# Kernel tuning notes

Measured on AMD Instinct MI355X. Metric: run time of the kernel, lower is better.

The kernel has to match this reference:

```python
import jax, jax.numpy as jnp
import numpy as np
from jax import lax

N_TOKENS = 524288
N_EXPERTS = 64
TOP_K = 8


def setup_inputs() -> dict:
    key = jax.random.key(0)
    logits = jax.random.normal(key, (N_TOKENS, N_EXPERTS), dtype=jnp.float32)
    # expert_counts / assignments / offsets are output buffers in the torch
    # module (filled by the custom kernel); pass zero placeholders.
    return {
        "expert_counts": jnp.zeros((N_EXPERTS,), dtype=jnp.int32),
        "assignments": jnp.zeros((N_TOKENS, TOP_K), dtype=jnp.int32),
        "offsets": jnp.zeros((N_TOKENS, TOP_K), dtype=jnp.int32),
        "logits": logits,
    }


def reference(expert_counts, assignments, offsets, logits):
    """Ragged top-k gating (replay_routing=False).

    Returns (expert_counts, scores, assignments, offsets, logits_out):
      scores       [N, K]  top-k softmax probabilities per token
      assignments  [N, K]  top-k expert ids per token
      offsets      [N, K]  slot of each (token, k) within its expert's
                           ragged bucket (token-major arrival order)
      expert_counts[E]     number of routed slots per expert
      logits_out           pass-through copy of logits
    """
    N, E = logits.shape
    K = assignments.shape[1]

    probs = jax.nn.softmax(logits, axis=-1)            # [N, E]
    scores, assign = lax.top_k(probs, K)               # [N, K] each
    assign = assign.astype(jnp.int32)

    flat = assign.reshape(-1)                          # [N*K], token-major
    counts = jnp.zeros((E,), jnp.int32).at[flat].add(1)

    # offsets: rank of each slot among equal-expert slots in arrival order.
    # Stable sort by expert id; within-expert rank = sorted position minus
    # the expert's segment start (exclusive cumsum of counts).
    order = jnp.argsort(flat, stable=True)             # [N*K]
    sorted_e = flat[order]
    starts = jnp.concatenate(
        [jnp.zeros((1,), jnp.int32), jnp.cumsum(counts)[:-1].astype(jnp.int32)]
    )                                                  # [E]
    ranks = jnp.arange(N * K, dtype=jnp.int32) - starts[sorted_e]
    offs = jnp.zeros((N * K,), jnp.int32).at[order].set(ranks).reshape(N, K)

    return counts, scores, assign, offs, logits
```

## Files before the change

kernel.cpp:

```cpp
#include <hip/hip_runtime.h>

#define NT 524288
#define NE 64
#define NK 8
#define TPB 128
#define NBLK (NT / TPB)
#define SPB (TPB * NK)

__global__ __launch_bounds__(256) void topk_kernel(
    const float* __restrict__ logits,
    float* __restrict__ out_scores,
    float* __restrict__ out_assign,
    float* __restrict__ out_logits,
    int* __restrict__ blockCounts)
{
    __shared__ int wcnt[4][NE];

    const int t = threadIdx.x;
    const int b = blockIdx.x;
    const int g = t & 7;
    const int tok_in_pass = t >> 3;
    const int w = t >> 6;
    const int l = t & 63;
    const unsigned long long lt_mask = (l == 0) ? 0ull : ((~0ull) >> (64 - l));

    int myCount = 0;

    for (int pass = 0; pass < 4; ++pass) {
        const int ltok = pass * 32 + tok_in_pass;
        const int token = b * TPB + ltok;
        const float* lp = logits + (size_t)token * NE + g * 8;
        float4 v0 = *(const float4*)lp;
        float4 v1 = *(const float4*)(lp + 4);
        float* op = out_logits + (size_t)token * NE + g * 8;
        *(float4*)op = v0;
        *(float4*)(op + 4) = v1;

        float lv[8] = {v0.x, v0.y, v0.z, v0.w, v1.x, v1.y, v1.z, v1.w};

        float m = lv[0];
        #pragma unroll
        for (int j = 1; j < 8; ++j) m = fmaxf(m, lv[j]);
        #pragma unroll
        for (int sh = 1; sh < 8; sh <<= 1) m = fmaxf(m, __shfl_xor(m, sh, 64));

        float p[8];
        float s = 0.f;
        #pragma unroll
        for (int j = 0; j < 8; ++j) { p[j] = expf(lv[j] - m); s += p[j]; }
        #pragma unroll
        for (int sh = 1; sh < 8; sh <<= 1) s += __shfl_xor(s, sh, 64);
        #pragma unroll
        for (int j = 0; j < 8; ++j) p[j] = p[j] / s;

        float sc = 0.f; int id = 0;
        #pragma unroll
        for (int k = 0; k < NK; ++k) {
            float bv = p[0]; int bi = 0;
            #pragma unroll
            for (int j = 1; j < 8; ++j)
                if (p[j] > bv) { bv = p[j]; bi = j; }
            int bidx = g * 8 + bi;
            #pragma unroll
            for (int sh = 1; sh < 8; sh <<= 1) {
                float ov = __shfl_xor(bv, sh, 64);
                int   oi = __shfl_xor(bidx, sh, 64);
                if (ov > bv || (ov == bv && oi < bidx)) { bv = ov; bidx = oi; }
            }
            if (g == k) { sc = bv; id = bidx; }
            if ((bidx >> 3) == g) p[bidx & 7] = -1.0f;
        }

        const size_t slot = (size_t)token * NK + g;
        out_scores[slot] = sc;
        out_assign[slot] = (float)id;

        const int e = id;
        unsigned long long mask = ~0ull;
        #pragma unroll
        for (int bit = 0; bit < 6; ++bit) {
            unsigned long long bb = __ballot((e >> bit) & 1);
            mask &= ((e >> bit) & 1) ? bb : ~bb;
        }
        wcnt[w][l] = 0;
        __syncthreads();
        if ((mask & lt_mask) == 0ull) wcnt[w][e] = __popcll(mask);
        __syncthreads();
        if (t < NE) myCount += wcnt[0][t] + wcnt[1][t] + wcnt[2][t] + wcnt[3][t];
        __syncthreads();
    }

    if (t < NE) blockCounts[b * NE + t] = myCount;
}

__global__ __launch_bounds__(256) void scan_kernel(
    int* __restrict__ blockCounts, float* __restrict__ out_counts)
{
    __shared__ int sdata[256];
    const int e = blockIdx.x;
    const int t = threadIdx.x;
    const int PER = NBLK / 256;

    int s = 0;
    for (int i = 0; i < PER; ++i) s += blockCounts[(t * PER + i) * NE + e];
    sdata[t] = s;
    __syncthreads();

    for (int off = 1; off < 256; off <<= 1) {
        int v = (t >= off) ? sdata[t - off] : 0;
        __syncthreads();
        sdata[t] += v;
        __syncthreads();
    }
    int run = (t == 0) ? 0 : sdata[t - 1];

    for (int i = 0; i < PER; ++i) {
        const int idx = (t * PER + i) * NE + e;
        const int c = blockCounts[idx];
        blockCounts[idx] = run;
        run += c;
    }
    if (t == 255) out_counts[e] = (float)sdata[255];
}

__global__ __launch_bounds__(256) void offs_kernel(
    const int* __restrict__ blockCounts,
    const float* __restrict__ out_assign,
    float* __restrict__ out_offs)
{
    __shared__ int running[NE];
    __shared__ int wcnt[4][NE];
    const int b = blockIdx.x;
    const int t = threadIdx.x;
    const int w = t >> 6;
    const int l = t & 63;
    const unsigned long long lt_mask = (l == 0) ? 0ull : ((~0ull) >> (64 - l));

    if (t < NE) running[t] = blockCounts[b * NE + t];

    #pragma unroll
    for (int tile = 0; tile < 4; ++tile) {
        const int gslot = b * SPB + tile * 256 + t;
        const int e = (int)out_assign[gslot];

        unsigned long long mask = ~0ull;
        #pragma unroll
        for (int bit = 0; bit < 6; ++bit) {
            unsigned long long bb = __ballot((e >> bit) & 1);
            mask &= ((e >> bit) & 1) ? bb : ~bb;
        }
        const int r_in_wave = __popcll(mask & lt_mask);
        const int wc = __popcll(mask);

        wcnt[w][l] = 0;
        __syncthreads();
        if ((mask & lt_mask) == 0ull) wcnt[w][e] = wc;
        __syncthreads();

        int before = running[e];
        for (int w2 = 0; w2 < w; ++w2) before += wcnt[w2][e];
        out_offs[gslot] = (float)(before + r_in_wave);

        __syncthreads();
        if (t < NE) running[t] += wcnt[0][t] + wcnt[1][t] + wcnt[2][t] + wcnt[3][t];
        __syncthreads();
    }
}

extern "C" void kernel_launch(void* const* d_in, const int* in_sizes, int n_in,
                              void* d_out, int out_size, void* d_ws, size_t ws_size,
                              hipStream_t stream) {
    const float* logits = (const float*)d_in[3];

    float* out = (float*)d_out;
    float* out_counts = out;
    float* out_scores = out + NE;
    float* out_assign = out_scores + (size_t)NT * NK;
    float* out_offs   = out_assign + (size_t)NT * NK;
    float* out_logits = out_offs + (size_t)NT * NK;

    int* blockCounts = (int*)d_ws;

    hipLaunchKernelGGL(topk_kernel, dim3(NBLK), dim3(256), 0, stream,
                       logits, out_scores, out_assign, out_logits, blockCounts);
    hipLaunchKernelGGL(scan_kernel, dim3(NE), dim3(256), 0, stream,
                       blockCounts, out_counts);
    hipLaunchKernelGGL(offs_kernel, dim3(NBLK), dim3(256), 0, stream,
                       blockCounts, out_assign, out_offs);
}
```

Before: 338.3 us.

## Remove per-pass barriers, transpose block counts, and stage scan through LDS

The top-k kernel now accumulates per-wave expert counts with LDS atomics across all passes, with a single barrier at the end instead of three barriers per pass. Block counts are stored expert-major, so the scan kernel can load each expert's column coalesced into padded shared memory and do a two-level scan there. The offsets kernel computes all four tiles' counts in one phase with one barrier, keeping expert ids and masks in registers. Occupancy hints are added to the launch bounds. This adds LDS atomics and more registers per thread, and makes the scan kernel's shared memory footprint larger.

Measured after the change: 328.6 us. -2.9%, faster.

```diff
diff --git a/kernel.cpp b/kernel.cpp
--- a/kernel.cpp
+++ b/kernel.cpp
@@ -7,7 +7,7 @@
 #define NBLK (NT / TPB)
 #define SPB (TPB * NK)
 
-__global__ __launch_bounds__(256) void topk_kernel(
+__global__ __launch_bounds__(256, 4) void topk_kernel(
     const float* __restrict__ logits,
     float* __restrict__ out_scores,
     float* __restrict__ out_assign,
@@ -24,8 +24,10 @@
     const int l = t & 63;
     const unsigned long long lt_mask = (l == 0) ? 0ull : ((~0ull) >> (64 - l));
 
-    int myCount = 0;
-
+    wcnt[w][l] = 0;
+    __syncthreads();
+
+    #pragma unroll
     for (int pass = 0; pass < 4; ++pass) {
         const int ltok = pass * 32 + tok_in_pass;
         const int token = b * TPB + ltok;
@@ -82,88 +84,117 @@
             unsigned long long bb = __ballot((e >> bit) & 1);
             mask &= ((e >> bit) & 1) ? bb : ~bb;
         }
-        wcnt[w][l] = 0;
-        __syncthreads();
-        if ((mask & lt_mask) == 0ull) wcnt[w][e] = __popcll(mask);
-        __syncthreads();
-        if (t < NE) myCount += wcnt[0][t] + wcnt[1][t] + wcnt[2][t] + wcnt[3][t];
-        __syncthreads();
-    }
-
-    if (t < NE) blockCounts[b * NE + t] = myCount;
+        if ((mask & lt_mask) == 0ull)
+            atomicAdd(&wcnt[w][e], __popcll(mask));
+    }
+
+    __syncthreads();
+    if (t < NE) {
+        const int c = wcnt[0][t] + wcnt[1][t] + wcnt[2][t] + wcnt[3][t];
+        blockCounts[t * NBLK + b] = c;
+    }
 }
 
 __global__ __launch_bounds__(256) void scan_kernel(
     int* __restrict__ blockCounts, float* __restrict__ out_counts)
 {
-    __shared__ int sdata[256];
+    __shared__ int buf[NBLK + (NBLK >> 4)];
+    __shared__ int part[256];
     const int e = blockIdx.x;
     const int t = threadIdx.x;
-    const int PER = NBLK / 256;
-
+    int* col = blockCounts + (size_t)e * NBLK;
+
+    #pragma unroll
+    for (int i = 0; i < 16; ++i) {
+        const int j = i * 256 + t;
+        buf[j + (j >> 4)] = col[j];
+    }
+    __syncthreads();
+
+    int loc[16];
     int s = 0;
-    for (int i = 0; i < PER; ++i) s += blockCounts[(t * PER + i) * NE + e];
-    sdata[t] = s;
+    #pragma unroll
+    for (int i = 0; i < 16; ++i) {
+        const int j = t * 16 + i;
+        loc[i] = s;
+        s += buf[j + (j >> 4)];
+    }
+    part[t] = s;
     __syncthreads();
 
     for (int off = 1; off < 256; off <<= 1) {
-        int v = (t >= off) ? sdata[t - off] : 0;
+        int v = (t >= off) ? part[t - off] : 0;
         __syncthreads();
-        sdata[t] += v;
+        part[t] += v;
         __syncthreads();
     }
-    int run = (t == 0) ? 0 : sdata[t - 1];
-
-    for (int i = 0; i < PER; ++i) {
-        const int idx = (t * PER + i) * NE + e;
-        const int c = blockCounts[idx];
-        blockCounts[idx] = run;
-        run += c;
-    }
-    if (t == 255) out_counts[e] = (float)sdata[255];
-}
-
-__global__ __launch_bounds__(256) void offs_kernel(
+    const int run = (t == 0) ? 0 : part[t - 1];
+
+    #pragma unroll
+    for (int i = 0; i < 16; ++i) {
+        const int j = t * 16 + i;
+        buf[j + (j >> 4)] = run + loc[i];
+    }
+    __syncthreads();
+    #pragma unroll
+    for (int i = 0; i < 16; ++i) {
+        const int j = i * 256 + t;
+        col[j] = buf[j + (j >> 4)];
+    }
+    if (t == 255) out_counts[e] = (float)part[255];
+}
+
+__global__ __launch_bounds__(256, 4) void offs_kernel(
     const int* __restrict__ blockCounts,
     const float* __restrict__ out_assign,
     float* __restrict__ out_offs)
 {
-    __shared__ int running[NE];
-    __shared__ int wcnt[4][NE];
+    __shared__ int cnt[4][4][NE];
+    __shared__ int base[NE];
+    const int t = threadIdx.x;
     const int b = blockIdx.x;
-    const int t = threadIdx.x;
     const int w = t >> 6;
     const int l = t & 63;
     const unsigned long long lt_mask = (l == 0) ? 0ull : ((~0ull) >> (64 - l));
 
-    if (t < NE) running[t] = blockCounts[b * NE + t];
-
-    #pragma unroll
-    for (int tile = 0; tile < 4; ++tile) {
-        const int gslot = b * SPB + tile * 256 + t;
+    #pragma unroll
+    for (int tau = 0; tau < 4; ++tau) cnt[tau][w][l] = 0;
+    if (t < NE) base[t] = blockCounts[t * NBLK + b];
+    __syncthreads();
+
+    int e_r[4];
+    unsigned long long mask_r[4];
+    #pragma unroll
+    for (int tau = 0; tau < 4; ++tau) {
+        const int gslot = b * SPB + tau * 256 + t;
         const int e = (int)out_assign[gslot];
-
+        e_r[tau] = e;
         unsigned long long mask = ~0ull;
         #pragma unroll
         for (int bit = 0; bit < 6; ++bit) {
             unsigned long long bb = __ballot((e >> bit) & 1);
             mask &= ((e >> bit) & 1) ? bb : ~bb;
         }
-        const int r_in_wave = __popcll(mask & lt_mask);
-        const int wc = __popcll(mask);
-
-        wcnt[w][l] = 0;
-        __syncthreads();
-        if ((mask & lt_mask) == 0ull) wcnt[w][e] = wc;
-        __syncthreads();
-
-        int before = running[e];
-        for (int w2 = 0; w2 < w; ++w2) before += wcnt[w2][e];
-        out_offs[gslot] = (float)(before + r_in_wave);
-
-        __syncthreads();
-        if (t < NE) running[t] += wcnt[0][t] + wcnt[1][t] + wcnt[2][t] + wcnt[3][t];
-        __syncthreads();
+        mask_r[tau] = mask;
+        if ((mask & lt_mask) == 0ull)
+            atomicAdd(&cnt[tau][w][e], __popcll(mask));
+    }
+    __syncthreads();
+
+    #pragma unroll
+    for (int tau = 0; tau < 4; ++tau) {
+        const int e = e_r[tau];
+        int before = base[e];
+        #pragma unroll
+        for (int tau2 = 0; tau2 < 4; ++tau2)
+            if (tau2 < tau)
+                before += cnt[tau2][0][e] + cnt[tau2][1][e]
+                        + cnt[tau2][2][e] + cnt[tau2][3][e];
+        if (w > 0) before += cnt[tau][0][e];
+        if (w > 1) before += cnt[tau][1][e];
+        if (w > 2) before += cnt[tau][2][e];
+        const int gslot = b * SPB + tau * 256 + t;
+        out_offs[gslot] = (float)(before + __popcll(mask_r[tau] & lt_mask));
     }
 }
 
```
